# Performance work log

Hardware: AMD Instinct MI355X
Metric: run time of the kernel (lower is better)

## Reference

```python
import jax, jax.numpy as jnp
import numpy as np

LN_EPS = 1e-5

def _layernorm(h, gamma, beta):
    mu = jnp.mean(h, axis=-1, keepdims=True)
    var = jnp.mean(jnp.square(h - mu), axis=-1, keepdims=True)
    return (h - mu) * jax.lax.rsqrt(var + LN_EPS) * gamma + beta

def setup_inputs() -> dict:
    key = jax.random.key(0)
    ks = jax.random.split(key, 8)
    B, T, D, H = 64, 512, 512, 1024
    x = jax.random.normal(ks[0], (B, T, D), dtype=jnp.float32)
    s_in = 1.0 / np.sqrt(D)
    s_h = 1.0 / np.sqrt(H)
    W_in = jax.random.uniform(ks[1], (H, D), minval=-s_in, maxval=s_in, dtype=jnp.float32)
    b_in = jax.random.uniform(ks[2], (H,), minval=-s_in, maxval=s_in, dtype=jnp.float32)
    W_state = jax.random.uniform(ks[3], (H, H), minval=-s_h, maxval=s_h, dtype=jnp.float32)
    b_state = jax.random.uniform(ks[4], (H,), minval=-s_h, maxval=s_h, dtype=jnp.float32)
    decay = jnp.zeros((H,), dtype=jnp.float32)  # nn.Parameter(torch.zeros(hidden))
    ln_gamma = jnp.ones((H,), dtype=jnp.float32)
    ln_beta = jnp.zeros((H,), dtype=jnp.float32)
    return {"x": x, "W_in": W_in, "b_in": b_in, "W_state": W_state,
            "b_state": b_state, "decay": decay, "ln_gamma": ln_gamma, "ln_beta": ln_beta}

def reference(x, W_in, b_in, W_state, b_state, decay, ln_gamma, ln_beta):
    B, T, D = x.shape
    H = W_in.shape[0]
    d = jax.nn.sigmoid(decay)  # [H]
    # Precompute the input drive for all steps: [B,T,H] -> time-major [T,B,H]
    u = jnp.einsum('btd,hd->bth', x, W_in) + b_in
    u = jnp.swapaxes(u, 0, 1)

    def step(state, u_t):
        driven = jnp.tanh(u_t + state @ W_state.T + b_state)
        state = d * state + (1.0 - d) * driven
        y = _layernorm(state, ln_gamma, ln_beta)
        return state, y

    init = jnp.zeros((B, H), dtype=x.dtype)
    _, ys = jax.lax.scan(step, init, u)  # ys: [T,B,H]
    return jnp.swapaxes(ys, 0, 1)  # [B,T,H]
```

## Files before the change

### kernel.cpp

```cpp
#include <hip/hip_runtime.h>
#include <hip/hip_bf16.h>


#define B_    64
#define T_    512
#define H_    1024
#define GCOLS 64

typedef __attribute__((ext_vector_type(8))) __bf16 bf16x8;
typedef __attribute__((ext_vector_type(4))) float f32x4;
typedef __attribute__((ext_vector_type(4))) unsigned uint32x4;

static __device__ __forceinline__ unsigned f2bf_bits(float f) {
    unsigned u = __float_as_uint(f);
    return (u + 0x7FFFu + ((u >> 16) & 1u)) >> 16;
}

static __device__ __forceinline__ float fast_tanh(float x) {
    x = fminf(fmaxf(x, -15.f), 15.f);
    const float e = __expf(2.f * x);
    return 1.f - 2.f * __builtin_amdgcn_rcpf(e + 1.f);
}

#define SLOADC(dst, base, BOFF)                                               \
    asm volatile("global_load_dwordx4 %0, %1, off offset:%2 sc0 sc1"          \
                 : "=&v"(dst) : "v"(base), "n"(BOFF))
#define ULOAD(dst, base)                                                      \
    asm volatile("global_load_dword %0, %1, off"                              \
                 : "=&v"(dst) : "v"(base))

#define BM 128
#define BN 128
#define BKK 32
#define LDT 40

__global__ __launch_bounds__(256)
void u_gemm(const float* __restrict__ X, const float* __restrict__ Win,
            const float* __restrict__ bin, float* __restrict__ U) {
    __shared__ unsigned short Al[BM][LDT];
    __shared__ unsigned short Bl[BN][LDT];
    const int tid = threadIdx.x;
    const int m0 = blockIdx.y * BM;
    const int n0 = blockIdx.x * BN;
    const int l  = tid & 63;
    const int w  = tid >> 6;
    const int wr = (w >> 1) * 64, wc = (w & 1) * 64;
    const int fr = l & 15, fk = (l >> 4) * 8;

    f32x4 acc[4][4];
#pragma unroll
    for (int m = 0; m < 4; ++m)
#pragma unroll
        for (int n = 0; n < 4; ++n) acc[m][n] = f32x4{0.f, 0.f, 0.f, 0.f};

    const int sr = tid >> 1;
    const int sc = (tid & 1) * 16;

    for (int k0 = 0; k0 < 512; k0 += BKK) {
        const float* ap = X   + (size_t)(m0 + sr) * 512 + k0 + sc;
        const float* bp = Win + (size_t)(n0 + sr) * 512 + k0 + sc;
        float a[16], b[16];
#pragma unroll
        for (int j = 0; j < 4; ++j) {
            *(float4*)&a[j * 4] = *(const float4*)(ap + j * 4);
            *(float4*)&b[j * 4] = *(const float4*)(bp + j * 4);
        }
        __syncthreads();
#pragma unroll
        for (int j = 0; j < 16; ++j) {
            Al[sr][sc + j] = (unsigned short)f2bf_bits(a[j]);
            Bl[sr][sc + j] = (unsigned short)f2bf_bits(b[j]);
        }
        __syncthreads();

        bf16x8 af[4], bf[4];
#pragma unroll
        for (int m = 0; m < 4; ++m)
            af[m] = *(const bf16x8*)&Al[wr + m * 16 + fr][fk];
#pragma unroll
        for (int n = 0; n < 4; ++n)
            bf[n] = *(const bf16x8*)&Bl[wc + n * 16 + fr][fk];
#pragma unroll
        for (int m = 0; m < 4; ++m)
#pragma unroll
            for (int n = 0; n < 4; ++n)
                acc[m][n] = __builtin_amdgcn_mfma_f32_16x16x32_bf16(
                    af[m], bf[n], acc[m][n], 0, 0, 0);
    }

#pragma unroll
    for (int m = 0; m < 4; ++m) {
#pragma unroll
        for (int n = 0; n < 4; ++n) {
            const int col = n0 + wc + n * 16 + fr;
            const float bb = bin[col];
#pragma unroll
            for (int r = 0; r < 4; ++r) {
                const int row = m0 + wr + m * 16 + (l >> 4) * 4 + r;
                U[(size_t)row * 1024 + col] = acc[m][n][r] + bb;
            }
        }
    }
}

__global__ __launch_bounds__(256, 1)
void rec_tag2(const float* __restrict__ Wst, float* __restrict__ UY,
              const float* __restrict__ b_state, const float* __restrict__ decay,
              const float* __restrict__ gamma, const float* __restrict__ beta,
              unsigned* __restrict__ Sbuf) {
    extern __shared__ __align__(16) unsigned char smem[];
    unsigned short* Wl = (unsigned short*)smem;
    unsigned*       Sl = (unsigned*)(smem + 131072);
    float*          muS = (float*)(smem + 131072);
    float*          rsS = muS + 16;

    const int tid  = threadIdx.x;
    const int bid  = blockIdx.x;
    const int rg   = bid >> 4;
    const int cbk  = bid & 15;
    const int h0   = cbk * GCOLS;
    const int wave = tid >> 6;
    const int lane = tid & 63;
    const int c    = lane & 15;
    const int rgrp = lane >> 4;
    const int mycol = h0 + wave * 16 + c;
    const int lrow  = wave * 4 + rgrp;

    {
        const int col = tid >> 2;
        const int sub = tid & 3;
        const float* wr_ = Wst + (size_t)(h0 + col) * H_ + sub * 256;
#pragma unroll
        for (int i = 0; i < 32; ++i) {
            float4 f0 = *(const float4*)(wr_ + i * 8);
            float4 f1 = *(const float4*)(wr_ + i * 8 + 4);
            unsigned short* dst = Wl + ((size_t)(sub * 32 + i) * 64 + col) * 8;
            dst[0] = (unsigned short)f2bf_bits(f0.x);
            dst[1] = (unsigned short)f2bf_bits(f0.y);
            dst[2] = (unsigned short)f2bf_bits(f0.z);
            dst[3] = (unsigned short)f2bf_bits(f0.w);
            dst[4] = (unsigned short)f2bf_bits(f1.x);
            dst[5] = (unsigned short)f2bf_bits(f1.y);
            dst[6] = (unsigned short)f2bf_bits(f1.z);
            dst[7] = (unsigned short)f2bf_bits(f1.w);
        }
    }

    const float d_c  = 1.f / (1.f + __expf(-decay[mycol]));
    const float od_c = 1.f - d_c;
    const float bs_c = b_state[mycol];
    const float g_c  = gamma[mycol];
    const float be_c = beta[mycol];

    float sold[4] = {0.f, 0.f, 0.f, 0.f};
    int brow[4];
#pragma unroll
    for (int r = 0; r < 4; ++r) brow[r] = rg * 16 + rgrp * 4 + r;

    float yv[4] = {0.f, 0.f, 0.f, 0.f};
    float uun[4], uu[4];
#pragma unroll
    for (int r = 0; r < 4; ++r)
        uun[r] = UY[(size_t)brow[r] * T_ * H_ + mycol];

    unsigned* const Sg = Sbuf + ((size_t)rg * 3 << 14);
    const int swzW = (lrow & 7) << 2;
    const int swzR = (c & 7) << 2;

    __syncthreads();

    for (int t = 0; t < T_; ++t) {
        const unsigned* Sr = Sg + ((size_t)(t % 3) << 14);
        unsigned*       Sw = Sg + ((size_t)((t + 1) % 3) << 14);
        const unsigned tagr = (unsigned)t, tagw = (unsigned)(t + 1);

        __syncthreads();

        asm volatile("" ::: "memory");
#pragma unroll
        for (int r = 0; r < 4; ++r) uu[r] = uun[r];

        uint32x4 tw[16];
        const unsigned* lb = Sr + (size_t)lrow * 1024 + c * 4;
#pragma unroll
        for (int j = 0; j < 16; ++j) SLOADC(tw[j], lb, j * 256);

        if (t >= 2) {
#pragma unroll
            for (int r = 0; r < 4; ++r)
                UY[((size_t)brow[r] * T_ + (t - 2)) * H_ + mycol] = yv[r];
        }
        {
            const int tn = (t + 1 < T_) ? (t + 1) : t;
#pragma unroll
            for (int r = 0; r < 4; ++r) {
                const float* ub = UY + ((size_t)brow[r] * T_ + tn) * H_ + mycol;
                ULOAD(uun[r], ub);
            }
        }

        int spin = 0;
        for (;;) {
            asm volatile("s_waitcnt vmcnt(0)" ::: "memory");
            __builtin_amdgcn_sched_barrier(0);
            unsigned mn = 0xFFFFFFFFu;
#pragma unroll
            for (int j = 0; j < 16; ++j) {
                unsigned m01 = tw[j][0] < tw[j][1] ? tw[j][0] : tw[j][1];
                unsigned m23 = tw[j][2] < tw[j][3] ? tw[j][2] : tw[j][3];
                unsigned m = m01 < m23 ? m01 : m23;
                mn = mn < m ? mn : m;
            }
            if (__all((mn >> 16) == tagr)) break;
            if (((++spin) & 7) == 7)
                __builtin_amdgcn_fence(__ATOMIC_ACQUIRE, "agent");
            __builtin_amdgcn_s_sleep(1);
#pragma unroll
            for (int j = 0; j < 16; ++j) SLOADC(tw[j], lb, j * 256);
        }

        float s1 = 0.f, s2 = 0.f;
#pragma unroll
        for (int j = 0; j < 16; ++j) {
#pragma unroll
            for (int k = 0; k < 4; ++k) {
                const float v = __uint_as_float(tw[j][k] << 16);
                s1 += v;
                s2 = fmaf(v, v, s2);
            }
        }
        s1 += __shfl_xor(s1, 1); s2 += __shfl_xor(s2, 1);
        s1 += __shfl_xor(s1, 2); s2 += __shfl_xor(s2, 2);
        s1 += __shfl_xor(s1, 4); s2 += __shfl_xor(s2, 4);
        s1 += __shfl_xor(s1, 8); s2 += __shfl_xor(s2, 8);
        const float mu_l = s1 * (1.f / (float)H_);
        const float rs_l = rsqrtf(s2 * (1.f / (float)H_) - mu_l * mu_l + 1e-5f);

#pragma unroll
        for (int j = 0; j < 16; ++j) {
            const unsigned p0 = __builtin_amdgcn_perm(tw[j][1], tw[j][0], 0x05040100u);
            const unsigned p1 = __builtin_amdgcn_perm(tw[j][3], tw[j][2], 0x05040100u);
            const int idx = (j * 32 + c * 2) ^ swzW;
            *(uint2*)&Sl[lrow * 512 + idx] = uint2{p0, p1};
        }
        __syncthreads();

        f32x4 a0 = {0.f, 0.f, 0.f, 0.f}, a1 = a0, a2 = a0, a3 = a0;
#pragma unroll
        for (int kk = 0; kk < 32; kk += 4) {
#pragma unroll
            for (int q = 0; q < 4; ++q) {
                const int ai = ((kk + q) * 16 + rgrp * 4) ^ swzR;
                const uint32x4 aw = *(const uint32x4*)&Sl[c * 512 + ai];
                const bf16x8 af = __builtin_bit_cast(bf16x8, aw);
                const bf16x8 bf = *(const bf16x8*)(Wl +
                    ((size_t)((kk + q) * 4 + rgrp) * 64 + wave * 16 + c) * 8);
                if (q == 0) a0 = __builtin_amdgcn_mfma_f32_16x16x32_bf16(af, bf, a0, 0, 0, 0);
                if (q == 1) a1 = __builtin_amdgcn_mfma_f32_16x16x32_bf16(af, bf, a1, 0, 0, 0);
                if (q == 2) a2 = __builtin_amdgcn_mfma_f32_16x16x32_bf16(af, bf, a2, 0, 0, 0);
                if (q == 3) a3 = __builtin_amdgcn_mfma_f32_16x16x32_bf16(af, bf, a3, 0, 0, 0);
            }
        }
        const f32x4 acc = (a0 + a1) + (a2 + a3);

        float sprev[4];
#pragma unroll
        for (int r = 0; r < 4; ++r) {
            sprev[r] = sold[r];
            const float pre = acc[r] + uu[r] + bs_c;
            const float sn  = d_c * sold[r] + od_c * fast_tanh(pre);
            sold[r] = sn;
            __hip_atomic_store(&Sw[(size_t)(rgrp * 4 + r) * 1024 + mycol],
                               (tagw << 16) | f2bf_bits(sn),
                               __ATOMIC_RELAXED, __HIP_MEMORY_SCOPE_AGENT);
        }

        __syncthreads();
        if (c == 0) { muS[lrow] = mu_l; rsS[lrow] = rs_l; }
        __syncthreads();
        if (t > 0) {
#pragma unroll
            for (int r = 0; r < 4; ++r) {
                const int R = rgrp * 4 + r;
                yv[r] = (sprev[r] - muS[R]) * rsS[R] * g_c + be_c;
            }
        }
    }

    {
#pragma unroll
        for (int r = 0; r < 4; ++r)
            UY[((size_t)brow[r] * T_ + (T_ - 2)) * H_ + mycol] = yv[r];

        const unsigned* Sr = Sg + ((size_t)(T_ % 3) << 14);
        const unsigned tagr = (unsigned)T_;
        uint32x4 tw[16];
        const unsigned* lb = Sr + (size_t)lrow * 1024 + c * 4;
        int spin = 0;
#pragma unroll
        for (int j = 0; j < 16; ++j) SLOADC(tw[j], lb, j * 256);
        for (;;) {
            asm volatile("s_waitcnt vmcnt(0)" ::: "memory");
            __builtin_amdgcn_sched_barrier(0);
            unsigned mn = 0xFFFFFFFFu;
#pragma unroll
            for (int j = 0; j < 16; ++j) {
                unsigned m01 = tw[j][0] < tw[j][1] ? tw[j][0] : tw[j][1];
                unsigned m23 = tw[j][2] < tw[j][3] ? tw[j][2] : tw[j][3];
                unsigned m = m01 < m23 ? m01 : m23;
                mn = mn < m ? mn : m;
            }
            if (__all((mn >> 16) == tagr)) break;
            if (((++spin) & 7) == 7)
                __builtin_amdgcn_fence(__ATOMIC_ACQUIRE, "agent");
            __builtin_amdgcn_s_sleep(1);
#pragma unroll
            for (int j = 0; j < 16; ++j) SLOADC(tw[j], lb, j * 256);
        }
        float s1 = 0.f, s2 = 0.f;
#pragma unroll
        for (int j = 0; j < 16; ++j) {
#pragma unroll
            for (int k = 0; k < 4; ++k) {
                const float v = __uint_as_float(tw[j][k] << 16);
                s1 += v;
                s2 = fmaf(v, v, s2);
            }
        }
        s1 += __shfl_xor(s1, 1); s2 += __shfl_xor(s2, 1);
        s1 += __shfl_xor(s1, 2); s2 += __shfl_xor(s2, 2);
        s1 += __shfl_xor(s1, 4); s2 += __shfl_xor(s2, 4);
        s1 += __shfl_xor(s1, 8); s2 += __shfl_xor(s2, 8);
        const float mu_l = s1 * (1.f / (float)H_);
        const float rs_l = rsqrtf(s2 * (1.f / (float)H_) - mu_l * mu_l + 1e-5f);
        __syncthreads();
        if (c == 0) { muS[lrow] = mu_l; rsS[lrow] = rs_l; }
        __syncthreads();
#pragma unroll
        for (int r = 0; r < 4; ++r) {
            const int R = rgrp * 4 + r;
            UY[((size_t)brow[r] * T_ + (T_ - 1)) * H_ + mycol] =
                (sold[r] - muS[R]) * rsS[R] * g_c + be_c;
        }
    }
}

extern "C" void kernel_launch(void* const* d_in, const int* in_sizes, int n_in,
                              void* d_out, int out_size, void* d_ws, size_t ws_size,
                              hipStream_t stream) {
    const float* x   = (const float*)d_in[0];
    const float* Win = (const float*)d_in[1];
    const float* bin = (const float*)d_in[2];
    const float* Wst = (const float*)d_in[3];
    const float* bst = (const float*)d_in[4];
    const float* dec = (const float*)d_in[5];
    const float* lng = (const float*)d_in[6];
    const float* lnb = (const float*)d_in[7];
    float* out = (float*)d_out;

    unsigned char* ws = (unsigned char*)d_ws;
    unsigned* Sbuf = (unsigned*)(ws + 4096);

    hipFuncSetAttribute(reinterpret_cast<const void*>(rec_tag2),
                        hipFuncAttributeMaxDynamicSharedMemorySize, 163840);

    hipMemsetAsync(Sbuf, 0, 4u * 3u * 16u * 1024u * 4u, stream);
    u_gemm<<<dim3(8, 256), 256, 0, stream>>>(x, Win, bin, out);
    rec_tag2<<<64, 256, 163840, stream>>>(Wst, out, bst, dec, lng, lnb, Sbuf);
}
```

Before: 1.893 ms.

## Replace per-element tagged state exchange with per-block flags and packed bf16 state

The recurrent kernel no longer stores a step tag in the upper half of each 32-bit state word. It writes plain bf16 state (half the bytes) and publishes a per-block step counter after a vmcnt wait and a barrier. Consumers spin on 16 flag words, then load the state once, which removes the repeated polling of the full 64 KB exchange tile. The cost is an extra flag round-trip and a serialised store-then-flag on each step's critical path.

```diff
diff --git a/kernel.cpp b/kernel.cpp
--- a/kernel.cpp
+++ b/kernel.cpp
@@ -15,6 +15,8 @@
     unsigned u = __float_as_uint(f);
     return (u + 0x7FFFu + ((u >> 16) & 1u)) >> 16;
 }
+static __device__ __forceinline__ float blo(unsigned v) { return __uint_as_float(v << 16); }
+static __device__ __forceinline__ float bhi(unsigned v) { return __uint_as_float(v & 0xFFFF0000u); }
 
 static __device__ __forceinline__ float fast_tanh(float x) {
     x = fminf(fmaxf(x, -15.f), 15.f);
@@ -25,6 +27,9 @@
 #define SLOADC(dst, base, BOFF)                                               \
     asm volatile("global_load_dwordx4 %0, %1, off offset:%2 sc0 sc1"          \
                  : "=&v"(dst) : "v"(base), "n"(BOFF))
+#define FLOADC(dst, base)                                                     \
+    asm volatile("global_load_dword %0, %1, off sc0 sc1"                      \
+                 : "=&v"(dst) : "v"(base))
 #define ULOAD(dst, base)                                                      \
     asm volatile("global_load_dword %0, %1, off"                              \
                  : "=&v"(dst) : "v"(base))
@@ -104,10 +109,10 @@
 }
 
 __global__ __launch_bounds__(256, 1)
-void rec_tag2(const float* __restrict__ Wst, float* __restrict__ UY,
+void rec_flag(const float* __restrict__ Wst, float* __restrict__ UY,
               const float* __restrict__ b_state, const float* __restrict__ decay,
               const float* __restrict__ gamma, const float* __restrict__ beta,
-              unsigned* __restrict__ Sbuf) {
+              unsigned short* __restrict__ Sbuf, unsigned* __restrict__ flags) {
     extern __shared__ __align__(16) unsigned char smem[];
     unsigned short* Wl = (unsigned short*)smem;
     unsigned*       Sl = (unsigned*)(smem + 131072);
@@ -163,28 +168,23 @@
     for (int r = 0; r < 4; ++r)
         uun[r] = UY[(size_t)brow[r] * T_ * H_ + mycol];
 
-    unsigned* const Sg = Sbuf + ((size_t)rg * 3 << 14);
+    unsigned short* const Sg = Sbuf + (size_t)rg * 3 * 16384;
+    const unsigned* const fp = flags + rg * 16 + (lane & 15);
     const int swzW = (lrow & 7) << 2;
     const int swzR = (c & 7) << 2;
 
     __syncthreads();
 
     for (int t = 0; t < T_; ++t) {
-        const unsigned* Sr = Sg + ((size_t)(t % 3) << 14);
-        unsigned*       Sw = Sg + ((size_t)((t + 1) % 3) << 14);
-        const unsigned tagr = (unsigned)t, tagw = (unsigned)(t + 1);
+        const unsigned short* Sr = Sg + (size_t)(t % 3) * 16384;
+        unsigned short*       Sw = Sg + (size_t)((t + 1) % 3) * 16384;
+        const unsigned tagr = (unsigned)t;
 
         __syncthreads();
 
         asm volatile("" ::: "memory");
 #pragma unroll
         for (int r = 0; r < 4; ++r) uu[r] = uun[r];
-
-        uint32x4 tw[16];
-        const unsigned* lb = Sr + (size_t)lrow * 1024 + c * 4;
-#pragma unroll
-        for (int j = 0; j < 16; ++j) SLOADC(tw[j], lb, j * 256);
-
         if (t >= 2) {
 #pragma unroll
             for (int r = 0; r < 4; ++r)
@@ -199,34 +199,36 @@
             }
         }
 
-        int spin = 0;
-        for (;;) {
-            asm volatile("s_waitcnt vmcnt(0)" ::: "memory");
-            __builtin_amdgcn_sched_barrier(0);
-            unsigned mn = 0xFFFFFFFFu;
-#pragma unroll
-            for (int j = 0; j < 16; ++j) {
-                unsigned m01 = tw[j][0] < tw[j][1] ? tw[j][0] : tw[j][1];
-                unsigned m23 = tw[j][2] < tw[j][3] ? tw[j][2] : tw[j][3];
-                unsigned m = m01 < m23 ? m01 : m23;
-                mn = mn < m ? mn : m;
-            }
-            if (__all((mn >> 16) == tagr)) break;
-            if (((++spin) & 7) == 7)
-                __builtin_amdgcn_fence(__ATOMIC_ACQUIRE, "agent");
-            __builtin_amdgcn_s_sleep(1);
-#pragma unroll
-            for (int j = 0; j < 16; ++j) SLOADC(tw[j], lb, j * 256);
-        }
+        {
+            int spin = 0;
+            for (;;) {
+                unsigned fv;
+                FLOADC(fv, fp);
+                asm volatile("s_waitcnt vmcnt(0)" ::: "memory");
+                __builtin_amdgcn_sched_barrier(0);
+                if (__ballot(fv >= tagr) == ~0ull) break;
+                if (((++spin) & 31) == 31)
+                    __builtin_amdgcn_fence(__ATOMIC_ACQUIRE, "agent");
+                __builtin_amdgcn_s_sleep(1);
+            }
+        }
+
+        uint32x4 tw[8];
+        const unsigned short* lb = Sr + (size_t)lrow * 1024 + c * 8;
+#pragma unroll
+        for (int j = 0; j < 8; ++j) SLOADC(tw[j], lb, j * 256);
+        asm volatile("s_waitcnt vmcnt(0)" ::: "memory");
+        __builtin_amdgcn_sched_barrier(0);
 
         float s1 = 0.f, s2 = 0.f;
 #pragma unroll
-        for (int j = 0; j < 16; ++j) {
+        for (int j = 0; j < 8; ++j) {
 #pragma unroll
             for (int k = 0; k < 4; ++k) {
-                const float v = __uint_as_float(tw[j][k] << 16);
-                s1 += v;
-                s2 = fmaf(v, v, s2);
+                const float e0 = blo(tw[j][k]), e1 = bhi(tw[j][k]);
+                s1 += e0 + e1;
+                s2 = fmaf(e0, e0, s2);
+                s2 = fmaf(e1, e1, s2);
             }
         }
         s1 += __shfl_xor(s1, 1); s2 += __shfl_xor(s2, 1);
@@ -237,11 +239,9 @@
         const float rs_l = rsqrtf(s2 * (1.f / (float)H_) - mu_l * mu_l + 1e-5f);
 
 #pragma unroll
-        for (int j = 0; j < 16; ++j) {
-            const unsigned p0 = __builtin_amdgcn_perm(tw[j][1], tw[j][0], 0x05040100u);
-            const unsigned p1 = __builtin_amdgcn_perm(tw[j][3], tw[j][2], 0x05040100u);
-            const int idx = (j * 32 + c * 2) ^ swzW;
-            *(uint2*)&Sl[lrow * 512 + idx] = uint2{p0, p1};
+        for (int j = 0; j < 8; ++j) {
+            const int idx = (j * 64 + c * 4) ^ swzW;
+            *(uint32x4*)&Sl[lrow * 512 + idx] = tw[j];
         }
         __syncthreads();
 
@@ -271,11 +271,15 @@
             const float sn  = d_c * sold[r] + od_c * fast_tanh(pre);
             sold[r] = sn;
             __hip_atomic_store(&Sw[(size_t)(rgrp * 4 + r) * 1024 + mycol],
-                               (tagw << 16) | f2bf_bits(sn),
+                               (unsigned short)f2bf_bits(sn),
                                __ATOMIC_RELAXED, __HIP_MEMORY_SCOPE_AGENT);
         }
 
-        __syncthreads();
+        asm volatile("s_waitcnt vmcnt(0)" ::: "memory");
+        __syncthreads();
+        if (tid == 0)
+            __hip_atomic_store(&flags[bid], (unsigned)(t + 1),
+                               __ATOMIC_RELAXED, __HIP_MEMORY_SCOPE_AGENT);
         if (c == 0) { muS[lrow] = mu_l; rsS[lrow] = rs_l; }
         __syncthreads();
         if (t > 0) {
@@ -292,39 +296,36 @@
         for (int r = 0; r < 4; ++r)
             UY[((size_t)brow[r] * T_ + (T_ - 2)) * H_ + mycol] = yv[r];
 
-        const unsigned* Sr = Sg + ((size_t)(T_ % 3) << 14);
+        const unsigned short* Sr = Sg + (size_t)(T_ % 3) * 16384;
         const unsigned tagr = (unsigned)T_;
-        uint32x4 tw[16];
-        const unsigned* lb = Sr + (size_t)lrow * 1024 + c * 4;
-        int spin = 0;
-#pragma unroll
-        for (int j = 0; j < 16; ++j) SLOADC(tw[j], lb, j * 256);
-        for (;;) {
-            asm volatile("s_waitcnt vmcnt(0)" ::: "memory");
-            __builtin_amdgcn_sched_barrier(0);
-            unsigned mn = 0xFFFFFFFFu;
-#pragma unroll
-            for (int j = 0; j < 16; ++j) {
-                unsigned m01 = tw[j][0] < tw[j][1] ? tw[j][0] : tw[j][1];
-                unsigned m23 = tw[j][2] < tw[j][3] ? tw[j][2] : tw[j][3];
-                unsigned m = m01 < m23 ? m01 : m23;
-                mn = mn < m ? mn : m;
-            }
-            if (__all((mn >> 16) == tagr)) break;
-            if (((++spin) & 7) == 7)
-                __builtin_amdgcn_fence(__ATOMIC_ACQUIRE, "agent");
-            __builtin_amdgcn_s_sleep(1);
-#pragma unroll
-            for (int j = 0; j < 16; ++j) SLOADC(tw[j], lb, j * 256);
-        }
+        {
+            int spin = 0;
+            for (;;) {
+                unsigned fv;
+                FLOADC(fv, fp);
+                asm volatile("s_waitcnt vmcnt(0)" ::: "memory");
+                __builtin_amdgcn_sched_barrier(0);
+                if (__ballot(fv >= tagr) == ~0ull) break;
+                if (((++spin) & 31) == 31)
+                    __builtin_amdgcn_fence(__ATOMIC_ACQUIRE, "agent");
+                __builtin_amdgcn_s_sleep(1);
+            }
+        }
+        uint32x4 tw[8];
+        const unsigned short* lb = Sr + (size_t)lrow * 1024 + c * 8;
+#pragma unroll
+        for (int j = 0; j < 8; ++j) SLOADC(tw[j], lb, j * 256);
+        asm volatile("s_waitcnt vmcnt(0)" ::: "memory");
+        __builtin_amdgcn_sched_barrier(0);
         float s1 = 0.f, s2 = 0.f;
 #pragma unroll
-        for (int j = 0; j < 16; ++j) {
+        for (int j = 0; j < 8; ++j) {
 #pragma unroll
             for (int k = 0; k < 4; ++k) {
-                const float v = __uint_as_float(tw[j][k] << 16);
-                s1 += v;
-                s2 = fmaf(v, v, s2);
+                const float e0 = blo(tw[j][k]), e1 = bhi(tw[j][k]);
+                s1 += e0 + e1;
+                s2 = fmaf(e0, e0, s2);
+                s2 = fmaf(e1, e1, s2);
             }
         }
         s1 += __shfl_xor(s1, 1); s2 += __shfl_xor(s2, 1);
@@ -359,12 +360,14 @@
     float* out = (float*)d_out;
 
     unsigned char* ws = (unsigned char*)d_ws;
-    unsigned* Sbuf = (unsigned*)(ws + 4096);
-
-    hipFuncSetAttribute(reinterpret_cast<const void*>(rec_tag2),
+    unsigned*       flags = (unsigned*)ws;
+    unsigned short* Sbuf  = (unsigned short*)(ws + 4096);
+
+    hipFuncSetAttribute(reinterpret_cast<const void*>(rec_flag),
                         hipFuncAttributeMaxDynamicSharedMemorySize, 163840);
 
-    hipMemsetAsync(Sbuf, 0, 4u * 3u * 16u * 1024u * 4u, stream);
+    hipMemsetAsync(ws, 0, 4096 + 4u * 3u * 16u * 1024u * 2u, stream);
     u_gemm<<<dim3(8, 256), 256, 0, stream>>>(x, Win, bin, out);
-    rec_tag2<<<64, 256, 163840, stream>>>(Wst, out, bst, dec, lng, lnb, Sbuf);
-}
+    rec_flag<<<64, 256, 163840, stream>>>(Wst, out, bst, dec, lng, lnb,
+                                          Sbuf, flags);
+}
```

New measurement: 1.975 ms. 1.04x slower.
